# Optimization experiments

Measured on AMD Instinct MI355X. Metric: run time of the kernel, lower is better.

## Reference

```python
import jax, jax.numpy as jnp
import numpy as np

B, S, D = 4, 2048, 2048
H, HD = 16, 128
MAX_SEQ = 2048


def setup_inputs() -> dict:
    key = jax.random.key(0)
    ks = jax.random.split(key, 6)
    scale = 1.0 / np.sqrt(D)
    h = jax.random.normal(ks[0], (B, S, D), dtype=jnp.float32)
    Wq = jax.random.normal(ks[1], (D, H * HD), dtype=jnp.float32) * scale
    Wk = jax.random.normal(ks[2], (D, H * HD), dtype=jnp.float32) * scale
    Wv = jax.random.normal(ks[3], (D, H * HD), dtype=jnp.float32) * scale
    Wo = jax.random.normal(ks[4], (H * HD, D), dtype=jnp.float32) * scale
    # torch Linear stores weight as [out, in]; keep that layout
    Wq, Wk, Wv, Wo = Wq.T, Wk.T, Wv.T, Wo.T
    K_cache = jnp.zeros((B, H, MAX_SEQ, HD), dtype=jnp.float32)
    V_cache = jnp.zeros((B, H, MAX_SEQ, HD), dtype=jnp.float32)
    # standard RoPE angles: theta = pos / 10000^(2i/hd)
    inv_freq = 1.0 / (10000.0 ** (np.arange(0, HD, 2, dtype=np.float32) / HD))
    t = np.arange(MAX_SEQ, dtype=np.float32)
    ang = np.outer(t, inv_freq)  # [MAX_SEQ, HD//2]
    freqs_cos = jnp.asarray(np.cos(ang), dtype=jnp.float32)
    freqs_sin = jnp.asarray(np.sin(ang), dtype=jnp.float32)
    return {"h": h, "Wq": Wq, "Wk": Wk, "Wv": Wv, "Wo": Wo,
            "K_cache": K_cache, "V_cache": V_cache,
            "freqs_cos": freqs_cos, "freqs_sin": freqs_sin, "pos": 0}


def _rope(x, cos, sin):
    # x: [B,H,S,HD]; cos/sin: [1,1,S,HD//2]; complex multiply on (even,odd) pairs
    xr = x.reshape(*x.shape[:-1], -1, 2)
    x0, x1 = xr[..., 0], xr[..., 1]
    out = jnp.stack([x0 * cos - x1 * sin, x0 * sin + x1 * cos], axis=-1)
    return out.reshape(x.shape)


def reference(h, Wq, Wk, Wv, Wo, K_cache, V_cache, freqs_cos, freqs_sin, pos):
    Bq, Sq, _ = h.shape
    Q = jnp.einsum('bsd,ed->bse', h, Wq).reshape(Bq, Sq, H, HD).transpose(0, 2, 1, 3)
    K = jnp.einsum('bsd,ed->bse', h, Wk).reshape(Bq, Sq, H, HD).transpose(0, 2, 1, 3)
    V = jnp.einsum('bsd,ed->bse', h, Wv).reshape(Bq, Sq, H, HD).transpose(0, 2, 1, 3)
    cos = freqs_cos[pos:pos + Sq][None, None]
    sin = freqs_sin[pos:pos + Sq][None, None]
    Q = _rope(Q, cos, sin)
    K = _rope(K, cos, sin)
    # KV-cache append then read back prefix
    K_full = jax.lax.dynamic_update_slice(K_cache, K, (0, 0, pos, 0))
    V_full = jax.lax.dynamic_update_slice(V_cache, V, (0, 0, pos, 0))
    L = pos + Sq
    K_all = K_full[:, :, :L]
    V_all = V_full[:, :, :L]
    scores = jnp.einsum('bhqd,bhkd->bhqk', Q, K_all) / jnp.sqrt(jnp.float32(HD))
    if Sq > 1:  # causal: query at absolute position pos+i attends keys <= pos+i
        mask = (pos + jnp.arange(Sq))[:, None] >= jnp.arange(L)[None, :]
        scores = jnp.where(mask[None, None], scores, jnp.float32(-1e30))
    attn = jax.nn.softmax(scores, axis=-1)
    out = jnp.einsum('bhqk,bhkd->bhqd', attn, V_all)
    out = out.transpose(0, 2, 1, 3).reshape(Bq, Sq, H * HD)
    return jnp.einsum('bse,de->bsd', out, Wo)
```

## Files before the change

kernel.cpp:

```cpp
#include <hip/hip_runtime.h>
#include <hip/hip_bf16.h>

typedef __attribute__((ext_vector_type(8))) short bf16x8;
typedef __attribute__((ext_vector_type(4))) float f32x4;
typedef __attribute__((ext_vector_type(4))) unsigned short u16x4;

#define BB 4
#define SS 2048
#define DD 2048
#define HH 16
#define HDD 128
#define MASKV (-30000.0f)
#define MINIT (-15000.0f)

__device__ __forceinline__ unsigned short f2bf(float f) {
  __hip_bfloat16 b = __float2bfloat16(f);
  return *reinterpret_cast<unsigned short*>(&b);
}
__device__ __forceinline__ void gl_lds16(const void* g, void* l) {
  __builtin_amdgcn_global_load_lds((const __attribute__((address_space(1))) unsigned int*)g,
                                   (__attribute__((address_space(3))) unsigned int*)l, 16, 0, 0);
}

__global__ __launch_bounds__(256) void convert_all(const float* __restrict__ h,
                                                   const float* __restrict__ Wq,
                                                   const float* __restrict__ Wk,
                                                   const float* __restrict__ Wv,
                                                   const float* __restrict__ Wo,
                                                   __hip_bfloat16* __restrict__ hb,
                                                   __hip_bfloat16* __restrict__ wqkv,
                                                   __hip_bfloat16* __restrict__ wo_b) {
  int blk = blockIdx.x;
  const float* src;
  __hip_bfloat16* dst;
  int base;
  if (blk < 16384)      { src = h;  dst = hb;             base = 0; }
  else if (blk < 20480) { src = Wq; dst = wqkv;           base = 16384; }
  else if (blk < 24576) { src = Wk; dst = wqkv + 4194304; base = 20480; }
  else if (blk < 28672) { src = Wv; dst = wqkv + 8388608; base = 24576; }
  else                  { src = Wo; dst = wo_b;           base = 28672; }
  int i = (blk - base) * 256 + threadIdx.x;
  f32x4 v = ((const f32x4*)src)[i];
  u16x4 o;
  o[0] = f2bf(v[0]); o[1] = f2bf(v[1]); o[2] = f2bf(v[2]); o[3] = f2bf(v[3]);
  ((u16x4*)dst)[i] = o;
}

template <int MODE>
__global__ __launch_bounds__(512, 1) void gemm256(const __hip_bfloat16* __restrict__ A,
                                                  const __hip_bfloat16* __restrict__ Bw,
                                                  __hip_bfloat16* __restrict__ Cbf,
                                                  __hip_bfloat16* __restrict__ Vt,
                                                  float* __restrict__ Cf,
                                                  const float* __restrict__ fc,
                                                  const float* __restrict__ fs,
                                                  const int* __restrict__ posp,
                                                  int M, int N, int K) {
  __shared__ __hip_bfloat16 As[2][2][128 * 64];
  __shared__ __hip_bfloat16 Bs[2][2][128 * 64];
  const int tid = threadIdx.x;
  const int wid = tid >> 6, lane = tid & 63;
  const int l15 = lane & 15, l4 = lane >> 4;
  const int wm = wid >> 2, wn = wid & 3;

  const int nbn = N >> 8;
  const int nb = (M >> 8) * nbn;
  const int bid = blockIdx.x;
  const int swz = (bid & 7) * (nb >> 3) + (bid >> 3);
  const int bm = swz / nbn, bn = swz % nbn;

  const int NT = K >> 6;

#define STAGE_HALF(Q, BUF, K0G)                                                   \
  {                                                                               \
    if ((Q) < 2) {                                                                \
      const long rowb = (long)bm * 256 + (Q) * 128;                               \
      _Pragma("unroll") for (int i = 0; i < 2; i++) {                             \
        int c = i * 512 + tid, rr = c >> 3, jj = (c & 7) ^ (rr & 7);              \
        gl_lds16(A + (rowb + rr) * (long)K + (K0G) + jj * 8,                      \
                 &As[BUF][(Q)][0] + c * 8);                                       \
      }                                                                           \
    } else {                                                                      \
      const long rowb = (long)bn * 256 + ((Q) - 2) * 128;                         \
      _Pragma("unroll") for (int i = 0; i < 2; i++) {                             \
        int c = i * 512 + tid, rr = c >> 3, jj = (c & 7) ^ (rr & 7);              \
        gl_lds16(Bw + (rowb + rr) * (long)K + (K0G) + jj * 8,                     \
                 &Bs[BUF][(Q) - 2][0] + c * 8);                                   \
      }                                                                           \
    }                                                                             \
  }

  f32x4 acc[8][4] = {};

#pragma unroll
  for (int q = 0; q < 4; ++q) STAGE_HALF(q, 0, 0);
#pragma unroll
  for (int q = 0; q < 4; ++q) STAGE_HALF(q, 1, 64);
  __syncthreads();

  for (int T = 0; T < NT; ++T) {
    const int cur = T & 1;
    const int nxt = cur ^ 1;
    const bool do_stage = (T >= 1) && (T + 1 < NT);
    const int k0n = (T + 1) << 6;

#pragma unroll
    for (int k2 = 0; k2 < 2; ++k2) {
      bf16x8 af[8], bg[4];
#pragma unroll
      for (int ni = 0; ni < 4; ni++) {
        int r = (wn & 1) * 64 + ni * 16 + l15;
        int j = (k2 * 4 + l4) ^ (r & 7);
        bg[ni] = *(const bf16x8*)(&Bs[cur][wn >> 1][0] + r * 64 + j * 8);
      }
#pragma unroll
      for (int mi = 0; mi < 8; mi++) {
        int r = mi * 16 + l15;
        int j = (k2 * 4 + l4) ^ (r & 7);
        af[mi] = *(const bf16x8*)(&As[cur][wm][0] + r * 64 + j * 8);
      }
      if (do_stage) {
        if (k2 == 0) { STAGE_HALF(0, nxt, k0n); STAGE_HALF(1, nxt, k0n); }
        else         { STAGE_HALF(2, nxt, k0n); STAGE_HALF(3, nxt, k0n); }
      }
      __builtin_amdgcn_s_setprio(1);
#pragma unroll
      for (int mi = 0; mi < 8; mi++)
#pragma unroll
        for (int ni = 0; ni < 4; ni++)
          acc[mi][ni] = __builtin_amdgcn_mfma_f32_16x16x32_bf16(af[mi], bg[ni],
                                                                acc[mi][ni], 0, 0, 0);
      __builtin_amdgcn_s_setprio(0);
    }
    asm volatile("s_waitcnt vmcnt(0)" ::: "memory");
    __builtin_amdgcn_s_barrier();
    asm volatile("" ::: "memory");
  }
#undef STAGE_HALF

  if (MODE == 0) {
    if (bn * 256 < 4096) {
      const int pos = *posp;
#pragma unroll
      for (int mi = 0; mi < 8; mi++)
#pragma unroll
        for (int ni = 0; ni < 4; ni++) {
          int n = bn * 256 + wn * 64 + ni * 16 + l15;
          int hd = n & 127;
          int ip = hd >> 1;
          bool odd = hd & 1;
#pragma unroll
          for (int r = 0; r < 4; r++) {
            float v = acc[mi][ni][r];
            float p = __shfl_xor(v, 1, 64);
            int m = bm * 256 + wm * 128 + mi * 16 + l4 * 4 + r;
            int s = m & (SS - 1);
            float cv = fc[(long)(pos + s) * 64 + ip];
            float sv = fs[(long)(pos + s) * 64 + ip];
            float out = odd ? (p * sv + v * cv) : (v * cv - p * sv);
            Cbf[(long)m * 4096 + n] = __float2bfloat16(out);
          }
        }
    } else {
#pragma unroll
      for (int mi = 0; mi < 8; mi++)
#pragma unroll
        for (int ni = 0; ni < 4; ni++) {
          int e = bn * 256 + wn * 64 + ni * 16 + l15 - 4096;
          int hh = e >> 7, hd = e & 127;
          int m0 = bm * 256 + wm * 128 + mi * 16 + l4 * 4;
          int b = m0 >> 11, s0 = m0 & (SS - 1);
          u16x4 pk;
#pragma unroll
          for (int r = 0; r < 4; r++) pk[r] = f2bf(acc[mi][ni][r]);
          *(u16x4*)(Vt + (((long)(b * HH + hh) * 128 + hd) * SS + s0)) = pk;
        }
    }
  } else {
#pragma unroll
    for (int mi = 0; mi < 8; mi++)
#pragma unroll
      for (int ni = 0; ni < 4; ni++) {
        int n = bn * 256 + wn * 64 + ni * 16 + l15;
#pragma unroll
        for (int r = 0; r < 4; r++) {
          int m = bm * 256 + wm * 128 + mi * 16 + l4 * 4 + r;
          Cf[(long)m * N + n] = acc[mi][ni][r];
        }
      }
  }
}

__global__ __launch_bounds__(256, 2) void attn_k(const __hip_bfloat16* __restrict__ qk,
                                                 const __hip_bfloat16* __restrict__ vt,
                                                 __hip_bfloat16* __restrict__ aout,
                                                 const int* __restrict__ posp) {
  __shared__ __hip_bfloat16 Ks[64 * 128];
  __shared__ __hip_bfloat16 Vs[128 * 64];
  __shared__ __hip_bfloat16 Ps[4][16 * 64];
  const int pos = *posp;
  const int orig = blockIdx.x;
  const int swz = (orig & 7) * 128 + (orig >> 3);
  const int qp = swz & 15, bh = swz >> 4;
  const int b = bh >> 4, h = bh & 15;
  const int tid = threadIdx.x;
  const int wave = tid >> 6, lane = tid & 63;
  const int l15 = lane & 15, l4 = lane >> 4;

  const long kbase = ((long)b * SS) * 4096 + 2048 + h * 128;
  const long vbase = ((long)bh * 128) * SS;
  const float sc2 = 0.08838834764831845f * 1.4426950408889634f;

  const int s_kr[4] = {(0 * 256 + tid) >> 4, (1 * 256 + tid) >> 4, (2 * 256 + tid) >> 4, (3 * 256 + tid) >> 4};
  const int s_kc = tid & 15;
  const int s_hd[4] = {(0 * 256 + tid) >> 3, (1 * 256 + tid) >> 3, (2 * 256 + tid) >> 3, (3 * 256 + tid) >> 3};
  const int s_vc = tid & 7;

  bf16x8 kreg[4], vreg[4];

#define LOADKV(T)                                                                             \
  {                                                                                           \
    const int kv0_ = (T) * 64;                                                                \
    _Pragma("unroll") for (int i = 0; i < 4; i++) {                                           \
      kreg[i] = *(const bf16x8*)(qk + kbase + (long)(kv0_ + s_kr[i]) * 4096 + s_kc * 8);      \
      vreg[i] = *(const bf16x8*)(vt + vbase + (long)s_hd[i] * SS + kv0_ + s_vc * 8);          \
    }                                                                                         \
  }

#define STAGE()                                                                               \
  {                                                                                           \
    _Pragma("unroll") for (int i = 0; i < 4; i++) {                                           \
      *(bf16x8*)(Ks + ((s_kr[i] * 128 + s_kc * 8) ^ ((s_kr[i] & 7) << 3))) = kreg[i];         \
      *(bf16x8*)(Vs + ((s_hd[i] * 64 + s_vc * 8) ^ ((s_hd[i] & 7) << 3))) = vreg[i];          \
    }                                                                                         \
  }

  for (int half = 0; half < 2; ++half) {
    const int qb = half ? (31 - qp) : qp;
    const int qwb = qb * 64 + wave * 16;

    bf16x8 qf[4];
#pragma unroll
    for (int kk = 0; kk < 4; kk++) {
      long row = (long)b * SS + qwb + l15;
      qf[kk] = *(const bf16x8*)(qk + row * 4096 + h * 128 + kk * 32 + l4 * 8);
    }

    f32x4 accO[8] = {};
    float mrun[4], lrun[4];
#pragma unroll
    for (int r = 0; r < 4; r++) { mrun[r] = MINIT; lrun[r] = 0.f; }

    int ntiles = (pos + qb * 64 + 63) / 64 + 1;
    if (ntiles > SS / 64) ntiles = SS / 64;
#define TT(t) (half ? (ntiles - 1 - (t)) : (t))

    LOADKV(TT(0));
    __syncthreads();
    STAGE();

    for (int t = 0; t < ntiles; ++t) {
      const int kv0 = TT(t) * 64;
      __syncthreads();
      if (t + 1 < ntiles) LOADKV(TT(t + 1));

      f32x4 sfr[4] = {};
      __builtin_amdgcn_s_setprio(1);
#pragma unroll
      for (int ni = 0; ni < 4; ni++) {
        const int key = ni * 16 + l15;
        const int sw = (key & 7) << 3;
#pragma unroll
        for (int kk = 0; kk < 4; kk++) {
          bf16x8 kf = *(const bf16x8*)(Ks + ((key * 128 + kk * 32 + l4 * 8) ^ sw));
          sfr[ni] = __builtin_amdgcn_mfma_f32_16x16x32_bf16(qf[kk], kf, sfr[ni], 0, 0, 0);
        }
      }
      __builtin_amdgcn_s_setprio(0);

      const bool needmask = (kv0 + 63) > (pos + qb * 64);
#pragma unroll
      for (int ni = 0; ni < 4; ni++)
#pragma unroll
        for (int r = 0; r < 4; r++) {
          float v = sfr[ni][r] * sc2;
          if (needmask) {
            int key = kv0 + ni * 16 + l15;
            int q = qwb + l4 * 4 + r;
            if (key > pos + q) v = MASKV;
          }
          sfr[ni][r] = v;
        }

      {
        f32x4 mx = sfr[0];
#pragma unroll
        for (int ni = 1; ni < 4; ni++)
#pragma unroll
          for (int r = 0; r < 4; r++) mx[r] = fmaxf(mx[r], sfr[ni][r]);
#pragma unroll
        for (int d = 1; d < 16; d <<= 1)
#pragma unroll
          for (int r = 0; r < 4; r++) mx[r] = fmaxf(mx[r], __shfl_xor(mx[r], d, 64));

        float growth = mx[0] - mrun[0];
#pragma unroll
        for (int r = 1; r < 4; r++) growth = fmaxf(growth, mx[r] - mrun[r]);
        if (!__all(growth <= 11.0f)) {
          float scal[4];
#pragma unroll
          for (int r = 0; r < 4; r++) {
            float mn = fmaxf(mrun[r], mx[r]);
            scal[r] = exp2f(mrun[r] - mn);
            mrun[r] = mn;
            lrun[r] *= scal[r];
          }
#pragma unroll
          for (int ni = 0; ni < 8; ni++)
#pragma unroll
            for (int r = 0; r < 4; r++) accO[ni][r] *= scal[r];
        }

#pragma unroll
        for (int ni = 0; ni < 4; ni++)
#pragma unroll
          for (int r = 0; r < 4; r++) {
            float p = exp2f(sfr[ni][r] - mrun[r]);
            lrun[r] += p;
            int prow = l4 * 4 + r;
            Ps[wave][(prow * 64 + ni * 16 + l15) ^ ((prow & 7) << 3)] = __float2bfloat16(p);
          }
      }

      __builtin_amdgcn_s_setprio(1);
#pragma unroll
      for (int kk = 0; kk < 2; kk++) {
        int prow = l15;
        bf16x8 pf = *(const bf16x8*)(Ps[wave] + ((prow * 64 + kk * 32 + l4 * 8) ^ ((prow & 7) << 3)));
#pragma unroll
        for (int ni = 0; ni < 8; ni++) {
          int hd = ni * 16 + l15;
          bf16x8 vf = *(const bf16x8*)(Vs + ((hd * 64 + kk * 32 + l4 * 8) ^ ((hd & 7) << 3)));
          accO[ni] = __builtin_amdgcn_mfma_f32_16x16x32_bf16(pf, vf, accO[ni], 0, 0, 0);
        }
      }
      __builtin_amdgcn_s_setprio(0);

      __syncthreads();
      if (t + 1 < ntiles) STAGE();
    }
#undef TT

#pragma unroll
    for (int d = 1; d < 16; d <<= 1)
#pragma unroll
      for (int r = 0; r < 4; r++) lrun[r] += __shfl_xor(lrun[r], d, 64);

    __hip_bfloat16* E = Ks + wave * 2048;
    {
      float inv[4];
#pragma unroll
      for (int r = 0; r < 4; r++) inv[r] = 1.0f / lrun[r];
#pragma unroll
      for (int ni = 0; ni < 8; ni++)
#pragma unroll
        for (int r = 0; r < 4; r++) {
          int row = l4 * 4 + r;
          E[(row * 128 + ni * 16 + l15) ^ ((row & 7) << 3)] =
              __float2bfloat16(accO[ni][r] * inv[r]);
        }
    }
    const long gb = ((long)b * SS + qwb) * 2048 + h * 128;
#pragma unroll
    for (int j = 0; j < 4; j++) {
      int row = j * 4 + l4;
      int c8 = l15 * 8;
      bf16x8 v = *(const bf16x8*)(E + ((row * 128 + c8) ^ ((row & 7) << 3)));
      *(bf16x8*)(aout + gb + (long)row * 2048 + c8) = v;
    }
  }
#undef LOADKV
#undef STAGE
}

extern "C" void kernel_launch(void* const* d_in, const int* in_sizes, int n_in,
                              void* d_out, int out_size, void* d_ws, size_t ws_size,
                              hipStream_t stream) {
  (void)in_sizes; (void)n_in; (void)out_size; (void)ws_size;
  const float* h  = (const float*)d_in[0];
  const float* Wq = (const float*)d_in[1];
  const float* Wk = (const float*)d_in[2];
  const float* Wv = (const float*)d_in[3];
  const float* Wo = (const float*)d_in[4];
  const float* fc = (const float*)d_in[7];
  const float* fs = (const float*)d_in[8];
  const int* pos  = (const int*)d_in[9];
  float* out = (float*)d_out;

  char* ws = (char*)d_ws;
  __hip_bfloat16* hb    = (__hip_bfloat16*)(ws);
  __hip_bfloat16* wqkv  = (__hip_bfloat16*)(ws + 33554432);
  __hip_bfloat16* wo_b  = (__hip_bfloat16*)(ws + 58720256);
  __hip_bfloat16* qkbuf = (__hip_bfloat16*)(ws + 67108864);
  __hip_bfloat16* vt    = (__hip_bfloat16*)(ws + 134217728);
  __hip_bfloat16* aout  = hb;

  convert_all<<<32768, 256, 0, stream>>>(h, Wq, Wk, Wv, Wo, hb, wqkv, wo_b);

  gemm256<0><<<768, 512, 0, stream>>>(hb, wqkv, qkbuf, vt, nullptr, fc, fs, pos,
                                      8192, 6144, 2048);

  attn_k<<<1024, 256, 0, stream>>>(qkbuf, vt, aout, pos);

  gemm256<1><<<256, 512, 0, stream>>>(aout, wo_b, nullptr, nullptr, out, nullptr,
                                      nullptr, nullptr, 8192, 2048, 2048);
}
```

Measured before the change: 458.4 us.

## Use 4-wave GEMM blocks with 128x128 warp tiles instead of 8 waves

```diff
diff --git a/kernel.cpp b/kernel.cpp
--- a/kernel.cpp
+++ b/kernel.cpp
@@ -47,7 +47,7 @@
 }
 
 template <int MODE>
-__global__ __launch_bounds__(512, 1) void gemm256(const __hip_bfloat16* __restrict__ A,
+__global__ __launch_bounds__(256, 1) void gemm256(const __hip_bfloat16* __restrict__ A,
                                                   const __hip_bfloat16* __restrict__ Bw,
                                                   __hip_bfloat16* __restrict__ Cbf,
                                                   __hip_bfloat16* __restrict__ Vt,
@@ -56,12 +56,12 @@
                                                   const float* __restrict__ fs,
                                                   const int* __restrict__ posp,
                                                   int M, int N, int K) {
-  __shared__ __hip_bfloat16 As[2][2][128 * 64];
-  __shared__ __hip_bfloat16 Bs[2][2][128 * 64];
+  __shared__ __hip_bfloat16 As[2][256 * 64];
+  __shared__ __hip_bfloat16 Bs[2][256 * 64];
   const int tid = threadIdx.x;
   const int wid = tid >> 6, lane = tid & 63;
   const int l15 = lane & 15, l4 = lane >> 4;
-  const int wm = wid >> 2, wn = wid & 3;
+  const int wm = wid >> 1, wn = wid & 1;
 
   const int nbn = N >> 8;
   const int nb = (M >> 8) * nbn;
@@ -71,31 +71,27 @@
 
   const int NT = K >> 6;
 
-#define STAGE_HALF(Q, BUF, K0G)                                                   \
+#define STAGE_A(BUF, K0G)                                                         \
   {                                                                               \
-    if ((Q) < 2) {                                                                \
-      const long rowb = (long)bm * 256 + (Q) * 128;                               \
-      _Pragma("unroll") for (int i = 0; i < 2; i++) {                             \
-        int c = i * 512 + tid, rr = c >> 3, jj = (c & 7) ^ (rr & 7);              \
-        gl_lds16(A + (rowb + rr) * (long)K + (K0G) + jj * 8,                      \
-                 &As[BUF][(Q)][0] + c * 8);                                       \
-      }                                                                           \
-    } else {                                                                      \
-      const long rowb = (long)bn * 256 + ((Q) - 2) * 128;                         \
-      _Pragma("unroll") for (int i = 0; i < 2; i++) {                             \
-        int c = i * 512 + tid, rr = c >> 3, jj = (c & 7) ^ (rr & 7);              \
-        gl_lds16(Bw + (rowb + rr) * (long)K + (K0G) + jj * 8,                     \
-                 &Bs[BUF][(Q) - 2][0] + c * 8);                                   \
-      }                                                                           \
+    _Pragma("unroll") for (int i = 0; i < 8; i++) {                               \
+      int c = i * 256 + tid, rr = c >> 3, jj = (c & 7) ^ (rr & 7);                \
+      gl_lds16(A + ((long)bm * 256 + rr) * K + (K0G) + jj * 8,                    \
+               &As[BUF][0] + c * 8);                                              \
     }                                                                             \
   }
-
-  f32x4 acc[8][4] = {};
-
-#pragma unroll
-  for (int q = 0; q < 4; ++q) STAGE_HALF(q, 0, 0);
-#pragma unroll
-  for (int q = 0; q < 4; ++q) STAGE_HALF(q, 1, 64);
+#define STAGE_B(BUF, K0G)                                                         \
+  {                                                                               \
+    _Pragma("unroll") for (int i = 0; i < 8; i++) {                               \
+      int c = i * 256 + tid, rr = c >> 3, jj = (c & 7) ^ (rr & 7);                \
+      gl_lds16(Bw + ((long)bn * 256 + rr) * K + (K0G) + jj * 8,                   \
+               &Bs[BUF][0] + c * 8);                                              \
+    }                                                                             \
+  }
+
+  f32x4 acc[8][8] = {};
+
+  STAGE_A(0, 0); STAGE_B(0, 0);
+  STAGE_A(1, 64); STAGE_B(1, 64);
   __syncthreads();
 
   for (int T = 0; T < NT; ++T) {
@@ -106,28 +102,28 @@
 
 #pragma unroll
     for (int k2 = 0; k2 < 2; ++k2) {
-      bf16x8 af[8], bg[4];
-#pragma unroll
-      for (int ni = 0; ni < 4; ni++) {
-        int r = (wn & 1) * 64 + ni * 16 + l15;
+      bf16x8 af[8], bg[8];
+#pragma unroll
+      for (int ni = 0; ni < 8; ni++) {
+        int r = wn * 128 + ni * 16 + l15;
         int j = (k2 * 4 + l4) ^ (r & 7);
-        bg[ni] = *(const bf16x8*)(&Bs[cur][wn >> 1][0] + r * 64 + j * 8);
+        bg[ni] = *(const bf16x8*)(&Bs[cur][0] + r * 64 + j * 8);
       }
 #pragma unroll
       for (int mi = 0; mi < 8; mi++) {
-        int r = mi * 16 + l15;
+        int r = wm * 128 + mi * 16 + l15;
         int j = (k2 * 4 + l4) ^ (r & 7);
-        af[mi] = *(const bf16x8*)(&As[cur][wm][0] + r * 64 + j * 8);
+        af[mi] = *(const bf16x8*)(&As[cur][0] + r * 64 + j * 8);
       }
       if (do_stage) {
-        if (k2 == 0) { STAGE_HALF(0, nxt, k0n); STAGE_HALF(1, nxt, k0n); }
-        else         { STAGE_HALF(2, nxt, k0n); STAGE_HALF(3, nxt, k0n); }
+        if (k2 == 0) { STAGE_A(nxt, k0n); }
+        else         { STAGE_B(nxt, k0n); }
       }
       __builtin_amdgcn_s_setprio(1);
 #pragma unroll
       for (int mi = 0; mi < 8; mi++)
 #pragma unroll
-        for (int ni = 0; ni < 4; ni++)
+        for (int ni = 0; ni < 8; ni++)
           acc[mi][ni] = __builtin_amdgcn_mfma_f32_16x16x32_bf16(af[mi], bg[ni],
                                                                 acc[mi][ni], 0, 0, 0);
       __builtin_amdgcn_s_setprio(0);
@@ -136,7 +132,8 @@
     __builtin_amdgcn_s_barrier();
     asm volatile("" ::: "memory");
   }
-#undef STAGE_HALF
+#undef STAGE_A
+#undef STAGE_B
 
   if (MODE == 0) {
     if (bn * 256 < 4096) {
@@ -144,8 +141,8 @@
 #pragma unroll
       for (int mi = 0; mi < 8; mi++)
 #pragma unroll
-        for (int ni = 0; ni < 4; ni++) {
-          int n = bn * 256 + wn * 64 + ni * 16 + l15;
+        for (int ni = 0; ni < 8; ni++) {
+          int n = bn * 256 + wn * 128 + ni * 16 + l15;
           int hd = n & 127;
           int ip = hd >> 1;
           bool odd = hd & 1;
@@ -165,8 +162,8 @@
 #pragma unroll
       for (int mi = 0; mi < 8; mi++)
 #pragma unroll
-        for (int ni = 0; ni < 4; ni++) {
-          int e = bn * 256 + wn * 64 + ni * 16 + l15 - 4096;
+        for (int ni = 0; ni < 8; ni++) {
+          int e = bn * 256 + wn * 128 + ni * 16 + l15 - 4096;
           int hh = e >> 7, hd = e & 127;
           int m0 = bm * 256 + wm * 128 + mi * 16 + l4 * 4;
           int b = m0 >> 11, s0 = m0 & (SS - 1);
@@ -180,8 +177,8 @@
 #pragma unroll
     for (int mi = 0; mi < 8; mi++)
 #pragma unroll
-      for (int ni = 0; ni < 4; ni++) {
-        int n = bn * 256 + wn * 64 + ni * 16 + l15;
+      for (int ni = 0; ni < 8; ni++) {
+        int n = bn * 256 + wn * 128 + ni * 16 + l15;
 #pragma unroll
         for (int r = 0; r < 4; r++) {
           int m = bm * 256 + wm * 128 + mi * 16 + l4 * 4 + r;
@@ -407,11 +404,11 @@
 
   convert_all<<<32768, 256, 0, stream>>>(h, Wq, Wk, Wv, Wo, hb, wqkv, wo_b);
 
-  gemm256<0><<<768, 512, 0, stream>>>(hb, wqkv, qkbuf, vt, nullptr, fc, fs, pos,
+  gemm256<0><<<768, 256, 0, stream>>>(hb, wqkv, qkbuf, vt, nullptr, fc, fs, pos,
                                       8192, 6144, 2048);
 
   attn_k<<<1024, 256, 0, stream>>>(qkbuf, vt, aout, pos);
 
-  gemm256<1><<<256, 512, 0, stream>>>(aout, wo_b, nullptr, nullptr, out, nullptr,
+  gemm256<1><<<256, 256, 0, stream>>>(aout, wo_b, nullptr, nullptr, out, nullptr,
                                       nullptr, nullptr, 8192, 2048, 2048);
 }
```

Measured after the change: 490.3 us. 1.07x slower.
